# Kernel tuning notes

Measured on AMD Instinct MI355X. Metric: run time of the kernel, lower is better.

The kernel has to match this reference:

```python
import jax, jax.numpy as jnp
import numpy as np

H = 8
SPLIT = 1
# deterministic stand-in for random.shuffle(range(8)) in the original
_PERM = np.random.RandomState(0).permutation(H)
SERIES_IDX = jnp.asarray(_PERM[SPLIT:])  # 7 heads
CROSS_IDX = jnp.asarray(_PERM[:SPLIT])   # 1 head


def setup_inputs() -> dict:
    key = jax.random.key(0)
    ks = jax.random.split(key, 5)
    B, L, E = 8, 1024, 64
    shp = (B, L, H, E)
    return {
        "queries": jax.random.normal(ks[0], shp, dtype=jnp.float32),
        "keys": jax.random.normal(ks[1], shp, dtype=jnp.float32),
        "keysT": jax.random.normal(ks[2], shp, dtype=jnp.float32),
        "values": jax.random.normal(ks[3], shp, dtype=jnp.float32),
        "valuesT": jax.random.normal(ks[4], shp, dtype=jnp.float32),
    }


def reference(queries, keys, keysT, values, valuesT):
    B, L, _, E = queries.shape
    scale = 1.0 / jnp.sqrt(jnp.asarray(E, dtype=queries.dtype))
    neg_inf = jnp.asarray(-jnp.inf, dtype=queries.dtype)

    # head split (gather along head dim)
    sq = queries[:, :, SERIES_IDX]   # [B,L,7,E]
    sk = keys[:, :, SERIES_IDX]      # [B,S,7,E]
    sv = values[:, :, SERIES_IDX]    # [B,S,7,D]
    cq = queries[:, :, CROSS_IDX]    # [B,L,1,E]
    ckT = keysT[:, :, CROSS_IDX]     # [B,C,1,E]
    cvT = valuesT[:, :, CROSS_IDX]   # [B,C,1,D]

    # causal mask: True above the diagonal -> disallowed
    causal = jnp.triu(jnp.ones((L, L), dtype=bool), k=1)  # [L,L]

    # series branch
    scores = jnp.einsum('blne,bsne->bnls', sq, sk)  # [B,7,L,S]
    scores = jnp.where(causal[None, None], neg_inf, scores * scale)
    series = jax.nn.softmax(scores, axis=-1)
    V = jnp.einsum('bhls,bshd->blhd', series, sv)   # [B,L,7,D]

    # cross branch
    cscores = jnp.einsum('blme,bcme->bmlc', cq, ckT)  # [B,1,L,C]
    cscores = jnp.where(causal[None, None], neg_inf, cscores * scale)
    crosses = jax.nn.softmax(cscores, axis=-1)
    V_cross = jnp.einsum('bhlc,bchd->blhd', crosses, cvT)  # [B,L,1,D]

    return jnp.concatenate([V, V_cross], axis=2)  # [B,L,8,D]
```

## Files before the change

kernel.cpp:

```cpp
#include <hip/hip_runtime.h>
#include <math.h>

#define Lq 1024
#define Hq 8
#define Eq 64
#define LDW 72
#define KV_SH (64 * LDW)
#define BUF_SH (2 * KV_SH)

#define SRC_HEAD_PACKED 0x64503712u

typedef __bf16 bf16_t;
typedef __bf16 bf16x8 __attribute__((ext_vector_type(8)));
typedef __bf16 bf16x4 __attribute__((ext_vector_type(4)));
typedef short short4v __attribute__((ext_vector_type(4)));
typedef float floatx4 __attribute__((ext_vector_type(4)));

__device__ __forceinline__ bf16x8 cvt8(const float4 a, const float4 b) {
    bf16x8 r;
    r[0] = (bf16_t)a.x; r[1] = (bf16_t)a.y; r[2] = (bf16_t)a.z; r[3] = (bf16_t)a.w;
    r[4] = (bf16_t)b.x; r[5] = (bf16_t)b.y; r[6] = (bf16_t)b.z; r[7] = (bf16_t)b.w;
    return r;
}

__device__ __forceinline__ void block_sync_lds() {
    asm volatile("s_waitcnt lgkmcnt(0)" ::: "memory");
    __builtin_amdgcn_s_barrier();
    __builtin_amdgcn_sched_barrier(0);
}

__global__ __launch_bounds__(512, 4)
void attn_mfma(const float* __restrict__ Q, const float* __restrict__ Ks,
               const float* __restrict__ KTs, const float* __restrict__ Vs,
               const float* __restrict__ VTs, float* __restrict__ out) {
    const int slot = blockIdx.x;
    const int b    = blockIdx.y;
    const int p    = blockIdx.z;
    const int h    = (SRC_HEAD_PACKED >> (slot * 4)) & 0xF;
    const float* __restrict__ Kp = (slot == 7) ? KTs : Ks;
    const float* __restrict__ Vp = (slot == 7) ? VTs : Vs;
    const int pA = p, pB = 15 - p;

    const int tid  = threadIdx.x;
    const int wv   = tid >> 6;
    const int lane = tid & 63;
    const int ln16 = lane & 15;
    const int quad = lane >> 4;
    const int tb   = wv >> 2;
    const int kh   = (wv >> 1) & 1;
    const int wh   = wv & 1;
    const int pT   = tb ? pB : pA;

    __shared__ alignas(16) unsigned short smem[2 * BUF_SH];

    const float qs = 0.125f * 1.44269504f;
    bf16x8 qf[2][2];
    #pragma unroll
    for (int qi = 0; qi < 2; ++qi) {
        const int qg = wh * 2 + qi;
        const int r = pT * 64 + qg * 16 + ln16;
        const float* qa = Q + (((size_t)b * Lq + r) * Hq + h) * Eq + quad * 8;
        #pragma unroll
        for (int ec = 0; ec < 2; ++ec) {
            float4 f0 = ((const float4*)(qa + ec * 32))[0];
            float4 f1 = ((const float4*)(qa + ec * 32))[1];
            f0.x*=qs; f0.y*=qs; f0.z*=qs; f0.w*=qs;
            f1.x*=qs; f1.y*=qs; f1.z*=qs; f1.w*=qs;
            qf[qi][ec] = cvt8(f0, f1);
        }
    }

    floatx4 O[2][4];
    #pragma unroll
    for (int qi = 0; qi < 2; ++qi)
        #pragma unroll
        for (int dc = 0; dc < 4; ++dc) O[qi][dc] = (floatx4){0, 0, 0, 0};
    float psl[2] = {0.f, 0.f};

    float4 kq[2];
    float  vq[8];
    const int kj = tid >> 3, kc = (tid & 7) * 8;
    const int vd = tid & 63, vk = (tid >> 6) * 8;

    auto load_tile = [&](int kt) {
        const float* kb = Kp + (((size_t)b * Lq + kt * 64 + kj) * Hq + h) * Eq + kc;
        kq[0] = ((const float4*)kb)[0]; kq[1] = ((const float4*)kb)[1];
        const float* vb = Vp + (((size_t)b * Lq + kt * 64 + vk) * Hq + h) * Eq + vd;
        #pragma unroll
        for (int i = 0; i < 8; ++i) vq[i] = vb[(size_t)i * (Hq * Eq)];
    };
    auto stage = [&](int bsel) {
        unsigned short* dst = smem + bsel * BUF_SH;
        *(bf16x8*)&dst[kj * LDW + kc] = cvt8(kq[0], kq[1]);
        const float4* vq4 = (const float4*)vq;
        *(bf16x8*)&dst[KV_SH + vd * LDW + vk] = cvt8(vq4[0], vq4[1]);
    };

    load_tile(0);
    stage(0);
    load_tile(1);
    block_sync_lds();

    for (int kt = 0; kt <= pB; ++kt) {
        const unsigned short* base = smem + (kt & 1) * BUF_SH;
        const bool act = (kt <= pT);

        bf16x8 kf[2][2];
        if (act) {
            #pragma unroll
            for (int c = 0; c < 2; ++c) {
                kf[c][0] = *(const bf16x8*)&base[((kh * 2 + c) * 16 + ln16) * LDW + quad * 8];
                kf[c][1] = *(const bf16x8*)&base[((kh * 2 + c) * 16 + ln16) * LDW + 32 + quad * 8];
            }
        }
        if (kt < pB) stage((kt + 1) & 1);
        if (kt + 1 < pB) load_tile(kt + 2);

        if (act) {
            bf16x4 va[4][2];
            #pragma unroll
            for (int dc = 0; dc < 4; ++dc)
                #pragma unroll
                for (int nc = 0; nc < 2; ++nc)
                    va[dc][nc] = *(const bf16x4*)&base[KV_SH + (dc * 16 + ln16) * LDW + kh * 32 + nc * 16 + quad * 4];

            const bool diag = (kt == pT);
            #pragma unroll
            for (int qi = 0; qi < 2; ++qi) {
                const int qg = wh * 2 + qi;
                if (diag && kh && wh == 0) continue;

                floatx4 s[2];
                #pragma unroll
                for (int nc = 0; nc < 2; ++nc) {
                    floatx4 acc = (floatx4){0, 0, 0, 0};
                    acc = __builtin_amdgcn_mfma_f32_16x16x32_bf16(kf[nc][0], qf[qi][0], acc, 0, 0, 0);
                    acc = __builtin_amdgcn_mfma_f32_16x16x32_bf16(kf[nc][1], qf[qi][1], acc, 0, 0, 0);
                    s[nc] = acc;
                }
                if (diag) {
                    const int rin = qg * 16 + ln16;
                    #pragma unroll
                    for (int nc = 0; nc < 2; ++nc)
                        #pragma unroll
                        for (int r = 0; r < 4; ++r)
                            if (kh * 32 + nc * 16 + quad * 4 + r > rin) s[nc][r] = -INFINITY;
                }
                float pv[2][4];
                float ps = 0.f;
                #pragma unroll
                for (int nc = 0; nc < 2; ++nc)
                    #pragma unroll
                    for (int r = 0; r < 4; ++r) {
                        pv[nc][r] = __builtin_amdgcn_exp2f(s[nc][r]);
                        ps += pv[nc][r];
                    }
                psl[qi] += ps;

                short4v pb[2];
                #pragma unroll
                for (int nc = 0; nc < 2; ++nc) {
                    bf16x4 t;
                    t[0] = (bf16_t)pv[nc][0]; t[1] = (bf16_t)pv[nc][1];
                    t[2] = (bf16_t)pv[nc][2]; t[3] = (bf16_t)pv[nc][3];
                    pb[nc] = __builtin_bit_cast(short4v, t);
                }
                #pragma unroll
                for (int dc = 0; dc < 4; ++dc)
                    #pragma unroll
                    for (int nc = 0; nc < 2; ++nc)
                        O[qi][dc] = __builtin_amdgcn_mfma_f32_16x16x16bf16_1k(
                            __builtin_bit_cast(short4v, va[dc][nc]), pb[nc], O[qi][dc], 0, 0, 0);
            }
        }
        block_sync_lds();
    }

    float lsum[2];
    #pragma unroll
    for (int qi = 0; qi < 2; ++qi) {
        float l = psl[qi];
        l += __shfl_xor(l, 16, 64);
        l += __shfl_xor(l, 32, 64);
        lsum[qi] = l;
    }

    float* mb = (float*)smem;
    if (kh) {
        #pragma unroll
        for (int qi = 0; qi < 2; ++qi) {
            const int qg = wh * 2 + qi;
            float* dst = mb + ((tb * 4 + qg) * 64 + lane) * 18;
            #pragma unroll
            for (int dc = 0; dc < 4; ++dc) {
                *(float2*)(dst + dc * 4)     = make_float2(O[qi][dc][0], O[qi][dc][1]);
                *(float2*)(dst + dc * 4 + 2) = make_float2(O[qi][dc][2], O[qi][dc][3]);
            }
            dst[16] = lsum[qi];
        }
    }
    __syncthreads();
    if (!kh) {
        #pragma unroll
        for (int qi = 0; qi < 2; ++qi) {
            const int qg = wh * 2 + qi;
            const float* src = mb + ((tb * 4 + qg) * 64 + lane) * 18;
            const float inv = 1.0f / (lsum[qi] + src[16]);
            const int row = pT * 64 + qg * 16 + ln16;
            float* op = out + (((size_t)b * Lq + row) * Hq + slot) * Eq + quad * 4;
            #pragma unroll
            for (int dc = 0; dc < 4; ++dc) {
                float4 o;
                o.x = (O[qi][dc][0] + src[dc * 4 + 0]) * inv;
                o.y = (O[qi][dc][1] + src[dc * 4 + 1]) * inv;
                o.z = (O[qi][dc][2] + src[dc * 4 + 2]) * inv;
                o.w = (O[qi][dc][3] + src[dc * 4 + 3]) * inv;
                *(float4*)(op + dc * 16) = o;
            }
        }
    }
}

extern "C" void kernel_launch(void* const* d_in, const int* in_sizes, int n_in,
                              void* d_out, int out_size, void* d_ws, size_t ws_size,
                              hipStream_t stream) {
    const float* queries = (const float*)d_in[0];
    const float* keys    = (const float*)d_in[1];
    const float* keysT   = (const float*)d_in[2];
    const float* values  = (const float*)d_in[3];
    const float* valuesT = (const float*)d_in[4];
    float* out = (float*)d_out;

    dim3 grid(Hq, 8, 8);
    dim3 block(512);
    attn_mfma<<<grid, block, 0, stream>>>(queries, keys, keysT, values, valuesT, out);
}
```

Baseline: 127.2 us.

## Stage two KV tiles per iteration to halve block barriers

```diff
diff --git a/kernel.cpp b/kernel.cpp
--- a/kernel.cpp
+++ b/kernel.cpp
@@ -7,6 +7,7 @@
 #define LDW 72
 #define KV_SH (64 * LDW)
 #define BUF_SH (2 * KV_SH)
+#define PAIR_SH (2 * BUF_SH)
 
 #define SRC_HEAD_PACKED 0x64503712u
 
@@ -51,7 +52,7 @@
     const int wh   = wv & 1;
     const int pT   = tb ? pB : pA;
 
-    __shared__ alignas(16) unsigned short smem[2 * BUF_SH];
+    __shared__ alignas(16) unsigned short smem[2 * PAIR_SH];
 
     const float qs = 0.125f * 1.44269504f;
     bf16x8 qf[2][2];
@@ -77,46 +78,61 @@
         for (int dc = 0; dc < 4; ++dc) O[qi][dc] = (floatx4){0, 0, 0, 0};
     float psl[2] = {0.f, 0.f};
 
-    float4 kq[2];
-    float  vq[8];
-    const int kj = tid >> 3, kc = (tid & 7) * 8;
-    const int vd = tid & 63, vk = (tid >> 6) * 8;
-
-    auto load_tile = [&](int kt) {
-        const float* kb = Kp + (((size_t)b * Lq + kt * 64 + kj) * Hq + h) * Eq + kc;
+    const int th = tid >> 8, rtid = tid & 255;
+    const int kj = rtid >> 2, kc = (rtid & 3) * 16;
+    const int vd = rtid & 63, vk = ((rtid >> 6) & 3) * 16;
+
+    float4 kq[4];
+    float  vq[16];
+
+    auto load2 = [&](int kt0) {
+        const int t = min(kt0 + th, 15);
+        const float* kb = Kp + (((size_t)b * Lq + t * 64 + kj) * Hq + h) * Eq + kc;
         kq[0] = ((const float4*)kb)[0]; kq[1] = ((const float4*)kb)[1];
-        const float* vb = Vp + (((size_t)b * Lq + kt * 64 + vk) * Hq + h) * Eq + vd;
-        #pragma unroll
-        for (int i = 0; i < 8; ++i) vq[i] = vb[(size_t)i * (Hq * Eq)];
+        kq[2] = ((const float4*)kb)[2]; kq[3] = ((const float4*)kb)[3];
+        const float* vb = Vp + (((size_t)b * Lq + t * 64 + vk) * Hq + h) * Eq + vd;
+        #pragma unroll
+        for (int i = 0; i < 16; ++i) vq[i] = vb[(size_t)i * (Hq * Eq)];
     };
     auto stage = [&](int bsel) {
-        unsigned short* dst = smem + bsel * BUF_SH;
-        *(bf16x8*)&dst[kj * LDW + kc] = cvt8(kq[0], kq[1]);
+        unsigned short* dst = smem + bsel * PAIR_SH + th * BUF_SH;
+        *(bf16x8*)&dst[kj * LDW + kc]     = cvt8(kq[0], kq[1]);
+        *(bf16x8*)&dst[kj * LDW + kc + 8] = cvt8(kq[2], kq[3]);
         const float4* vq4 = (const float4*)vq;
-        *(bf16x8*)&dst[KV_SH + vd * LDW + vk] = cvt8(vq4[0], vq4[1]);
+        *(bf16x8*)&dst[KV_SH + vd * LDW + vk]     = cvt8(vq4[0], vq4[1]);
+        *(bf16x8*)&dst[KV_SH + vd * LDW + vk + 8] = cvt8(vq4[2], vq4[3]);
     };
 
-    load_tile(0);
+    const int nIt = (pB + 2) >> 1;
+
+    load2(0);
     stage(0);
-    load_tile(1);
+    load2(2);
     block_sync_lds();
 
-    for (int kt = 0; kt <= pB; ++kt) {
-        const unsigned short* base = smem + (kt & 1) * BUF_SH;
-        const bool act = (kt <= pT);
-
-        bf16x8 kf[2][2];
-        if (act) {
-            #pragma unroll
-            for (int c = 0; c < 2; ++c) {
-                kf[c][0] = *(const bf16x8*)&base[((kh * 2 + c) * 16 + ln16) * LDW + quad * 8];
-                kf[c][1] = *(const bf16x8*)&base[((kh * 2 + c) * 16 + ln16) * LDW + 32 + quad * 8];
-            }
-        }
-        if (kt < pB) stage((kt + 1) & 1);
-        if (kt + 1 < pB) load_tile(kt + 2);
-
-        if (act) {
+    for (int it = 0; it < nIt; ++it) {
+        const unsigned short* pbase = smem + (it & 1) * PAIR_SH;
+
+        #pragma unroll
+        for (int s2 = 0; s2 < 2; ++s2) {
+            const int ktile = 2 * it + s2;
+            const bool act = (ktile <= pT);
+            const unsigned short* base = pbase + s2 * BUF_SH;
+
+            bf16x8 kf[2][2];
+            if (act) {
+                #pragma unroll
+                for (int c = 0; c < 2; ++c) {
+                    kf[c][0] = *(const bf16x8*)&base[((kh * 2 + c) * 16 + ln16) * LDW + quad * 8];
+                    kf[c][1] = *(const bf16x8*)&base[((kh * 2 + c) * 16 + ln16) * LDW + 32 + quad * 8];
+                }
+            }
+            if (s2 == 0) {
+                if (it + 1 < nIt) stage((it + 1) & 1);
+                if (it + 2 < nIt) load2(2 * (it + 2));
+            }
+            if (!act) continue;
+
             bf16x4 va[4][2];
             #pragma unroll
             for (int dc = 0; dc < 4; ++dc)
@@ -124,7 +140,7 @@
                 for (int nc = 0; nc < 2; ++nc)
                     va[dc][nc] = *(const bf16x4*)&base[KV_SH + (dc * 16 + ln16) * LDW + kh * 32 + nc * 16 + quad * 4];
 
-            const bool diag = (kt == pT);
+            const bool diag = (ktile == pT);
             #pragma unroll
             for (int qi = 0; qi < 2; ++qi) {
                 const int qg = wh * 2 + qi;
```

After: 154.4 us. +21.4%, slower.

## Process two KV tiles per barrier with paired double-buffered LDS staging

Applied to the files above, without the earlier changes.

```diff
diff --git a/kernel.cpp b/kernel.cpp
--- a/kernel.cpp
+++ b/kernel.cpp
@@ -7,6 +7,7 @@
 #define LDW 72
 #define KV_SH (64 * LDW)
 #define BUF_SH (2 * KV_SH)
+#define PAIR_SH (2 * BUF_SH)
 
 #define SRC_HEAD_PACKED 0x64503712u
 
@@ -51,7 +52,7 @@
     const int wh   = wv & 1;
     const int pT   = tb ? pB : pA;
 
-    __shared__ alignas(16) unsigned short smem[2 * BUF_SH];
+    __shared__ alignas(16) unsigned short smem[2 * PAIR_SH];
 
     const float qs = 0.125f * 1.44269504f;
     bf16x8 qf[2][2];
@@ -89,89 +90,98 @@
         #pragma unroll
         for (int i = 0; i < 8; ++i) vq[i] = vb[(size_t)i * (Hq * Eq)];
     };
-    auto stage = [&](int bsel) {
-        unsigned short* dst = smem + bsel * BUF_SH;
+    auto stage = [&](int bsel, int s2) {
+        unsigned short* dst = smem + bsel * PAIR_SH + s2 * BUF_SH;
         *(bf16x8*)&dst[kj * LDW + kc] = cvt8(kq[0], kq[1]);
         const float4* vq4 = (const float4*)vq;
         *(bf16x8*)&dst[KV_SH + vd * LDW + vk] = cvt8(vq4[0], vq4[1]);
     };
 
+    const int nIt = (pB + 2) >> 1;
+
     load_tile(0);
-    stage(0);
+    stage(0, 0);
     load_tile(1);
+    stage(0, 1);
     block_sync_lds();
 
-    for (int kt = 0; kt <= pB; ++kt) {
-        const unsigned short* base = smem + (kt & 1) * BUF_SH;
-        const bool act = (kt <= pT);
-
-        bf16x8 kf[2][2];
-        if (act) {
-            #pragma unroll
-            for (int c = 0; c < 2; ++c) {
-                kf[c][0] = *(const bf16x8*)&base[((kh * 2 + c) * 16 + ln16) * LDW + quad * 8];
-                kf[c][1] = *(const bf16x8*)&base[((kh * 2 + c) * 16 + ln16) * LDW + 32 + quad * 8];
-            }
-        }
-        if (kt < pB) stage((kt + 1) & 1);
-        if (kt + 1 < pB) load_tile(kt + 2);
-
-        if (act) {
-            bf16x4 va[4][2];
-            #pragma unroll
-            for (int dc = 0; dc < 4; ++dc)
+    for (int it = 0; it < nIt; ++it) {
+        const unsigned short* pbase = smem + (it & 1) * PAIR_SH;
+        const int nxt = (it + 1) & 1;
+        const bool pre = (it + 1 < nIt);
+
+        #pragma unroll
+        for (int s2 = 0; s2 < 2; ++s2) {
+            const int ktile = 2 * it + s2;
+            const bool act = (ktile <= pT);
+            const unsigned short* base = pbase + s2 * BUF_SH;
+
+            if (pre) load_tile(2 * (it + 1) + s2);
+
+            if (act) {
+                bf16x8 kf[2][2];
                 #pragma unroll
-                for (int nc = 0; nc < 2; ++nc)
-                    va[dc][nc] = *(const bf16x4*)&base[KV_SH + (dc * 16 + ln16) * LDW + kh * 32 + nc * 16 + quad * 4];
-
-            const bool diag = (kt == pT);
-            #pragma unroll
-            for (int qi = 0; qi < 2; ++qi) {
-                const int qg = wh * 2 + qi;
-                if (diag && kh && wh == 0) continue;
-
-                floatx4 s[2];
+                for (int c = 0; c < 2; ++c) {
+                    kf[c][0] = *(const bf16x8*)&base[((kh * 2 + c) * 16 + ln16) * LDW + quad * 8];
+                    kf[c][1] = *(const bf16x8*)&base[((kh * 2 + c) * 16 + ln16) * LDW + 32 + quad * 8];
+                }
+                bf16x4 va[4][2];
                 #pragma unroll
-                for (int nc = 0; nc < 2; ++nc) {
-                    floatx4 acc = (floatx4){0, 0, 0, 0};
-                    acc = __builtin_amdgcn_mfma_f32_16x16x32_bf16(kf[nc][0], qf[qi][0], acc, 0, 0, 0);
-                    acc = __builtin_amdgcn_mfma_f32_16x16x32_bf16(kf[nc][1], qf[qi][1], acc, 0, 0, 0);
-                    s[nc] = acc;
-                }
-                if (diag) {
-                    const int rin = qg * 16 + ln16;
+                for (int dc = 0; dc < 4; ++dc)
+                    #pragma unroll
+                    for (int nc = 0; nc < 2; ++nc)
+                        va[dc][nc] = *(const bf16x4*)&base[KV_SH + (dc * 16 + ln16) * LDW + kh * 32 + nc * 16 + quad * 4];
+
+                const bool diag = (ktile == pT);
+                #pragma unroll
+                for (int qi = 0; qi < 2; ++qi) {
+                    const int qg = wh * 2 + qi;
+                    if (diag && kh && wh == 0) continue;
+
+                    floatx4 s[2];
+                    #pragma unroll
+                    for (int nc = 0; nc < 2; ++nc) {
+                        floatx4 acc = (floatx4){0, 0, 0, 0};
+                        acc = __builtin_amdgcn_mfma_f32_16x16x32_bf16(kf[nc][0], qf[qi][0], acc, 0, 0, 0);
+                        acc = __builtin_amdgcn_mfma_f32_16x16x32_bf16(kf[nc][1], qf[qi][1], acc, 0, 0, 0);
+                        s[nc] = acc;
+                    }
+                    if (diag) {
+                        const int rin = qg * 16 + ln16;
+                        #pragma unroll
+                        for (int nc = 0; nc < 2; ++nc)
+                            #pragma unroll
+                            for (int r = 0; r < 4; ++r)
+                                if (kh * 32 + nc * 16 + quad * 4 + r > rin) s[nc][r] = -INFINITY;
+                    }
+                    float pv[2][4];
+                    float ps = 0.f;
                     #pragma unroll
                     for (int nc = 0; nc < 2; ++nc)
                         #pragma unroll
-                        for (int r = 0; r < 4; ++r)
-                            if (kh * 32 + nc * 16 + quad * 4 + r > rin) s[nc][r] = -INFINITY;
+                        for (int r = 0; r < 4; ++r) {
+                            pv[nc][r] = __builtin_amdgcn_exp2f(s[nc][r]);
+                            ps += pv[nc][r];
+                        }
+                    psl[qi] += ps;
+
+                    short4v pb[2];
+                    #pragma unroll
+                    for (int nc = 0; nc < 2; ++nc) {
+                        bf16x4 t;
+                        t[0] = (bf16_t)pv[nc][0]; t[1] = (bf16_t)pv[nc][1];
+                        t[2] = (bf16_t)pv[nc][2]; t[3] = (bf16_t)pv[nc][3];
+                        pb[nc] = __builtin_bit_cast(short4v, t);
+                    }
+                    #pragma unroll
+                    for (int dc = 0; dc < 4; ++dc)
+                        #pragma unroll
+                        for (int nc = 0; nc < 2; ++nc)
+                            O[qi][dc] = __builtin_amdgcn_mfma_f32_16x16x16bf16_1k(
+                                __builtin_bit_cast(short4v, va[dc][nc]), pb[nc], O[qi][dc], 0, 0, 0);
                 }
-                float pv[2][4];
-                float ps = 0.f;
-                #pragma unroll
-                for (int nc = 0; nc < 2; ++nc)
-                    #pragma unroll
-                    for (int r = 0; r < 4; ++r) {
-                        pv[nc][r] = __builtin_amdgcn_exp2f(s[nc][r]);
-                        ps += pv[nc][r];
-                    }
-                psl[qi] += ps;
-
-                short4v pb[2];
-                #pragma unroll
-                for (int nc = 0; nc < 2; ++nc) {
-                    bf16x4 t;
-                    t[0] = (bf16_t)pv[nc][0]; t[1] = (bf16_t)pv[nc][1];
-                    t[2] = (bf16_t)pv[nc][2]; t[3] = (bf16_t)pv[nc][3];
-                    pb[nc] = __builtin_bit_cast(short4v, t);
-                }
-                #pragma unroll
-                for (int dc = 0; dc < 4; ++dc)
-                    #pragma unroll
-                    for (int nc = 0; nc < 2; ++nc)
-                        O[qi][dc] = __builtin_amdgcn_mfma_f32_16x16x16bf16_1k(
-                            __builtin_bit_cast(short4v, va[dc][nc]), pb[nc], O[qi][dc], 0, 0, 0);
             }
+            if (pre) stage(nxt, s2);
         }
         block_sync_lds();
     }
```

Result: slower. 133.7 us (+5.2%).

## Pre-convert K/V to bf16 workspace and run LDS-free attention kernel

Applied to the files above, without the earlier changes.

```diff
diff --git a/kernel.cpp b/kernel.cpp
--- a/kernel.cpp
+++ b/kernel.cpp
@@ -4,11 +4,11 @@
 #define Lq 1024
 #define Hq 8
 #define Eq 64
-#define LDW 72
-#define KV_SH (64 * LDW)
-#define BUF_SH (2 * KV_SH)
 
 #define SRC_HEAD_PACKED 0x64503712u
+
+#define KW_ELEMS (8u * 8u * 1024u * 64u)
+#define WS_NEEDED ((size_t)2 * KW_ELEMS * sizeof(unsigned short))
 
 typedef __bf16 bf16_t;
 typedef __bf16 bf16x8 __attribute__((ext_vector_type(8)));
@@ -22,6 +22,206 @@
     r[4] = (bf16_t)b.x; r[5] = (bf16_t)b.y; r[6] = (bf16_t)b.z; r[7] = (bf16_t)b.w;
     return r;
 }
+
+__global__ __launch_bounds__(256, 2)
+void prep_kv(const float* __restrict__ Ks, const float* __restrict__ KTs,
+             const float* __restrict__ Vs, const float* __restrict__ VTs,
+             unsigned short* __restrict__ Kw, unsigned short* __restrict__ Vw) {
+    const int slot = blockIdx.x, b = blockIdx.y, lt = blockIdx.z;
+    const int h = (SRC_HEAD_PACKED >> (slot * 4)) & 0xF;
+    const float* __restrict__ Kp = (slot == 7) ? KTs : Ks;
+    const float* __restrict__ Vp = (slot == 7) ? VTs : Vs;
+    const int tid = threadIdx.x;
+    const int row = tid >> 2, c0 = (tid & 3) * 16;
+
+    {
+        const float* kb = Kp + (((size_t)b * Lq + lt * 64 + row) * Hq + h) * Eq + c0;
+        float4 f0 = ((const float4*)kb)[0], f1 = ((const float4*)kb)[1];
+        float4 f2 = ((const float4*)kb)[2], f3 = ((const float4*)kb)[3];
+        unsigned short* kd = Kw + (((size_t)slot * 8 + b) * Lq + lt * 64 + row) * Eq + c0;
+        *(bf16x8*)kd       = cvt8(f0, f1);
+        *(bf16x8*)(kd + 8) = cvt8(f2, f3);
+    }
+    __shared__ float vt[64][68];
+    {
+        const float* vb = Vp + (((size_t)b * Lq + lt * 64 + row) * Hq + h) * Eq + c0;
+        *(float4*)&vt[row][c0]      = ((const float4*)vb)[0];
+        *(float4*)&vt[row][c0 + 4]  = ((const float4*)vb)[1];
+        *(float4*)&vt[row][c0 + 8]  = ((const float4*)vb)[2];
+        *(float4*)&vt[row][c0 + 12] = ((const float4*)vb)[3];
+    }
+    __syncthreads();
+    {
+        const int d = row, l0 = c0;
+        float4 g0, g1, g2, g3;
+        g0.x = vt[l0 +  0][d]; g0.y = vt[l0 +  1][d]; g0.z = vt[l0 +  2][d]; g0.w = vt[l0 +  3][d];
+        g1.x = vt[l0 +  4][d]; g1.y = vt[l0 +  5][d]; g1.z = vt[l0 +  6][d]; g1.w = vt[l0 +  7][d];
+        g2.x = vt[l0 +  8][d]; g2.y = vt[l0 +  9][d]; g2.z = vt[l0 + 10][d]; g2.w = vt[l0 + 11][d];
+        g3.x = vt[l0 + 12][d]; g3.y = vt[l0 + 13][d]; g3.z = vt[l0 + 14][d]; g3.w = vt[l0 + 15][d];
+        unsigned short* vd = Vw + (((size_t)slot * 8 + b) * Eq + d) * Lq + lt * 64 + l0;
+        *(bf16x8*)vd       = cvt8(g0, g1);
+        *(bf16x8*)(vd + 8) = cvt8(g2, g3);
+    }
+}
+
+__global__ __launch_bounds__(256, 2)
+void attn_ws(const float* __restrict__ Q, const unsigned short* __restrict__ Kw,
+             const unsigned short* __restrict__ Vw, float* __restrict__ out) {
+    const int slot = blockIdx.x;
+    const int b    = blockIdx.y;
+    const int qt   = 15 - blockIdx.z;
+    const int h    = (SRC_HEAD_PACKED >> (slot * 4)) & 0xF;
+
+    const int tid  = threadIdx.x;
+    const int wv   = tid >> 6;
+    const int lane = tid & 63;
+    const int ln16 = lane & 15;
+    const int quad = lane >> 4;
+    const int qh   = wv >> 1;
+    const int kh   = wv & 1;
+
+    __shared__ float mb[4 * 64 * 18];
+
+    const float qs = 0.125f * 1.44269504f;
+    bf16x8 qf[2][2];
+    #pragma unroll
+    for (int qi = 0; qi < 2; ++qi) {
+        const int qg = qh * 2 + qi;
+        const int r = qt * 64 + qg * 16 + ln16;
+        const float* qa = Q + (((size_t)b * Lq + r) * Hq + h) * Eq + quad * 8;
+        #pragma unroll
+        for (int ec = 0; ec < 2; ++ec) {
+            float4 f0 = ((const float4*)(qa + ec * 32))[0];
+            float4 f1 = ((const float4*)(qa + ec * 32))[1];
+            f0.x*=qs; f0.y*=qs; f0.z*=qs; f0.w*=qs;
+            f1.x*=qs; f1.y*=qs; f1.z*=qs; f1.w*=qs;
+            qf[qi][ec] = cvt8(f0, f1);
+        }
+    }
+
+    floatx4 O[2][4];
+    #pragma unroll
+    for (int qi = 0; qi < 2; ++qi)
+        #pragma unroll
+        for (int dc = 0; dc < 4; ++dc) O[qi][dc] = (floatx4){0, 0, 0, 0};
+    float psl[2] = {0.f, 0.f};
+
+    const unsigned short* kbase = Kw + ((size_t)slot * 8 + b) * Lq * Eq + (size_t)kh * 32 * Eq;
+    const unsigned short* vbase = Vw + ((size_t)slot * 8 + b) * Eq * Lq + kh * 32;
+
+    for (int kt = 0; kt <= qt; ++kt) {
+        bf16x8 kf[2][2];
+        #pragma unroll
+        for (int c = 0; c < 2; ++c) {
+            const unsigned short* kr = kbase + ((size_t)kt * 64 + c * 16 + ln16) * Eq;
+            kf[c][0] = *(const bf16x8*)&kr[quad * 8];
+            kf[c][1] = *(const bf16x8*)&kr[32 + quad * 8];
+        }
+        bf16x4 va[4][2];
+        #pragma unroll
+        for (int dc = 0; dc < 4; ++dc) {
+            const unsigned short* vr = vbase + ((size_t)(dc * 16 + ln16)) * Lq + kt * 64;
+            #pragma unroll
+            for (int nc = 0; nc < 2; ++nc)
+                va[dc][nc] = *(const bf16x4*)&vr[nc * 16 + quad * 4];
+        }
+
+        const bool diag = (kt == qt);
+        #pragma unroll
+        for (int qi = 0; qi < 2; ++qi) {
+            const int qg = qh * 2 + qi;
+            if (diag && kh && qh == 0) continue;
+
+            floatx4 s[2];
+            #pragma unroll
+            for (int nc = 0; nc < 2; ++nc) {
+                floatx4 acc = (floatx4){0, 0, 0, 0};
+                acc = __builtin_amdgcn_mfma_f32_16x16x32_bf16(kf[nc][0], qf[qi][0], acc, 0, 0, 0);
+                acc = __builtin_amdgcn_mfma_f32_16x16x32_bf16(kf[nc][1], qf[qi][1], acc, 0, 0, 0);
+                s[nc] = acc;
+            }
+            if (diag) {
+                const int rin = qg * 16 + ln16;
+                #pragma unroll
+                for (int nc = 0; nc < 2; ++nc)
+                    #pragma unroll
+                    for (int r = 0; r < 4; ++r)
+                        if (kh * 32 + nc * 16 + quad * 4 + r > rin) s[nc][r] = -INFINITY;
+            }
+            float pv[2][4];
+            float ps = 0.f;
+            #pragma unroll
+            for (int nc = 0; nc < 2; ++nc)
+                #pragma unroll
+                for (int r = 0; r < 4; ++r) {
+                    pv[nc][r] = __builtin_amdgcn_exp2f(s[nc][r]);
+                    ps += pv[nc][r];
+                }
+            psl[qi] += ps;
+
+            short4v pb[2];
+            #pragma unroll
+            for (int nc = 0; nc < 2; ++nc) {
+                bf16x4 t;
+                t[0] = (bf16_t)pv[nc][0]; t[1] = (bf16_t)pv[nc][1];
+                t[2] = (bf16_t)pv[nc][2]; t[3] = (bf16_t)pv[nc][3];
+                pb[nc] = __builtin_bit_cast(short4v, t);
+            }
+            #pragma unroll
+            for (int dc = 0; dc < 4; ++dc)
+                #pragma unroll
+                for (int nc = 0; nc < 2; ++nc)
+                    O[qi][dc] = __builtin_amdgcn_mfma_f32_16x16x16bf16_1k(
+                        __builtin_bit_cast(short4v, va[dc][nc]), pb[nc], O[qi][dc], 0, 0, 0);
+        }
+    }
+
+    float lsum[2];
+    #pragma unroll
+    for (int qi = 0; qi < 2; ++qi) {
+        float l = psl[qi];
+        l += __shfl_xor(l, 16, 64);
+        l += __shfl_xor(l, 32, 64);
+        lsum[qi] = l;
+    }
+    if (kh) {
+        #pragma unroll
+        for (int qi = 0; qi < 2; ++qi) {
+            const int qg = qh * 2 + qi;
+            float* dst = mb + (qg * 64 + lane) * 18;
+            #pragma unroll
+            for (int dc = 0; dc < 4; ++dc) {
+                *(float2*)(dst + dc * 4)     = make_float2(O[qi][dc][0], O[qi][dc][1]);
+                *(float2*)(dst + dc * 4 + 2) = make_float2(O[qi][dc][2], O[qi][dc][3]);
+            }
+            dst[16] = lsum[qi];
+        }
+    }
+    __syncthreads();
+    if (!kh) {
+        #pragma unroll
+        for (int qi = 0; qi < 2; ++qi) {
+            const int qg = qh * 2 + qi;
+            const float* src = mb + (qg * 64 + lane) * 18;
+            const float inv = 1.0f / (lsum[qi] + src[16]);
+            const int row = qt * 64 + qg * 16 + ln16;
+            float* op = out + (((size_t)b * Lq + row) * Hq + slot) * Eq + quad * 4;
+            #pragma unroll
+            for (int dc = 0; dc < 4; ++dc) {
+                float4 o;
+                o.x = (O[qi][dc][0] + src[dc * 4 + 0]) * inv;
+                o.y = (O[qi][dc][1] + src[dc * 4 + 1]) * inv;
+                o.z = (O[qi][dc][2] + src[dc * 4 + 2]) * inv;
+                o.w = (O[qi][dc][3] + src[dc * 4 + 3]) * inv;
+                *(float4*)(op + dc * 16) = o;
+            }
+        }
+    }
+}
+
+#define LDW 72
+#define KV_SH (64 * LDW)
+#define BUF_SH (2 * KV_SH)
 
 __device__ __forceinline__ void block_sync_lds() {
     asm volatile("s_waitcnt lgkmcnt(0)" ::: "memory");
@@ -129,7 +329,6 @@
             for (int qi = 0; qi < 2; ++qi) {
                 const int qg = wh * 2 + qi;
                 if (diag && kh && wh == 0) continue;
-
                 floatx4 s[2];
                 #pragma unroll
                 for (int nc = 0; nc < 2; ++nc) {
@@ -156,7 +355,6 @@
                         ps += pv[nc][r];
                     }
                 psl[qi] += ps;
-
                 short4v pb[2];
                 #pragma unroll
                 for (int nc = 0; nc < 2; ++nc) {
@@ -184,13 +382,12 @@
         l += __shfl_xor(l, 32, 64);
         lsum[qi] = l;
     }
-
-    float* mb = (float*)smem;
+    float* mbf = (float*)smem;
     if (kh) {
         #pragma unroll
         for (int qi = 0; qi < 2; ++qi) {
             const int qg = wh * 2 + qi;
-            float* dst = mb + ((tb * 4 + qg) * 64 + lane) * 18;
+            float* dst = mbf + ((tb * 4 + qg) * 64 + lane) * 18;
             #pragma unroll
             for (int dc = 0; dc < 4; ++dc) {
                 *(float2*)(dst + dc * 4)     = make_float2(O[qi][dc][0], O[qi][dc][1]);
@@ -204,7 +401,7 @@
         #pragma unroll
         for (int qi = 0; qi < 2; ++qi) {
             const int qg = wh * 2 + qi;
-            const float* src = mb + ((tb * 4 + qg) * 64 + lane) * 18;
+            const float* src = mbf + ((tb * 4 + qg) * 64 + lane) * 18;
             const float inv = 1.0f / (lsum[qi] + src[16]);
             const int row = pT * 64 + qg * 16 + ln16;
             float* op = out + (((size_t)b * Lq + row) * Hq + slot) * Eq + quad * 4;
@@ -231,7 +428,16 @@
     const float* valuesT = (const float*)d_in[4];
     float* out = (float*)d_out;
 
-    dim3 grid(Hq, 8, 8);
-    dim3 block(512);
-    attn_mfma<<<grid, block, 0, stream>>>(queries, keys, keysT, values, valuesT, out);
-}
+    if (d_ws != nullptr && ws_size >= WS_NEEDED) {
+        unsigned short* Kw = (unsigned short*)d_ws;
+        unsigned short* Vw = Kw + KW_ELEMS;
+        dim3 grid(Hq, 8, 16);
+        dim3 block(256);
+        prep_kv<<<grid, block, 0, stream>>>(keys, keysT, values, valuesT, Kw, Vw);
+        attn_ws<<<grid, block, 0, stream>>>(queries, Kw, Vw, out);
+    } else {
+        dim3 grid(Hq, 8, 8);
+        dim3 block(512);
+        attn_mfma<<<grid, block, 0, stream>>>(queries, keys, keysT, values, valuesT, out);
+    }
+}
```

Result: slower. 169.5 us (+33.3%).
